# Optimization experiments

Hardware: AMD Instinct MI355X
Metric: run time of the kernel (lower is better)

## Reference

```python
import jax, jax.numpy as jnp
import numpy as np

B, L, K, D, S = 8, 1024, 1024, 128, 16  # batch, nodes, eigvecs, d_model(=d_inner), d_state
ABAR_EPS = 1e-3
BN_EPS = 1e-5


def setup_inputs() -> dict:
    key = jax.random.key(0)
    ks = jax.random.split(key, 10)
    x = jax.random.normal(ks[0], (B, L, D), jnp.float32)
    attn_mask = jnp.ones((B, L), jnp.bool_)
    EigVecs = jax.random.normal(ks[1], (B, L, K), jnp.float32)
    EigVals = jax.random.uniform(ks[2], (B, K), jnp.float32)
    # BatchNorm1d (eval mode) params
    bn_gamma = jnp.ones((D,), jnp.float32)
    bn_beta = jnp.zeros((D,), jnp.float32)
    bn_mean = jnp.zeros((D,), jnp.float32)
    bn_var = jnp.ones((D,), jnp.float32)
    # in_proj Linear(D, 2*D)
    W_in = jax.random.normal(ks[3], (D, 2 * D), jnp.float32) / np.float32(np.sqrt(D))
    b_in = jnp.zeros((2 * D,), jnp.float32)
    # SSM params
    log_Delta = np.float32(np.log(1e-3)) + np.float32(np.log(0.1) - np.log(1e-3)) * jax.random.uniform(ks[4], (1, D), jnp.float32)
    Bp = 0.01 * jax.random.normal(ks[5], (1, D, S), jnp.float32)
    Cp = 0.01 * jax.random.normal(ks[6], (1, D, S), jnp.float32)
    log_A_real = jnp.log(0.5 * jnp.ones((D, S), jnp.float32))
    A_imag = jnp.pi * jnp.broadcast_to(jnp.arange(D, dtype=jnp.float32)[:, None], (D, S))
    # out_proj Linear(D, D)
    W_out = jax.random.normal(ks[7], (D, D), jnp.float32) / np.float32(np.sqrt(D))
    b_out = jnp.zeros((D,), jnp.float32)
    return {
        "x": x, "attn_mask": attn_mask, "EigVecs": EigVecs, "EigVals": EigVals,
        "bn_gamma": bn_gamma, "bn_beta": bn_beta, "bn_mean": bn_mean, "bn_var": bn_var,
        "W_in": W_in, "b_in": b_in, "log_Delta": log_Delta, "Bp": Bp, "Cp": Cp,
        "log_A_real": log_A_real, "A_imag": A_imag, "W_out": W_out, "b_out": b_out,
    }


def reference(x, attn_mask, EigVecs, EigVals, bn_gamma, bn_beta, bn_mean, bn_var,
              W_in, b_in, log_Delta, Bp, Cp, log_A_real, A_imag, W_out, b_out):
    # --- eig preprocessing ---
    ev = 1.0 - EigVals[:, :, None, None]            # (B,K,1,1)
    ev = jnp.nan_to_num(ev)
    Q = jnp.nan_to_num(EigVecs)                      # (B,L,K)
    Q = Q / jnp.linalg.norm(Q, axis=-1, keepdims=True)
    Q = jnp.nan_to_num(Q)
    # --- in_proj: BatchNorm1d (eval) + Linear ---
    xb = (x - bn_mean) * (bn_gamma / jnp.sqrt(bn_var + BN_EPS)) + bn_beta
    h = xb @ W_in + b_in                             # (B,L,2D)
    x1, z = jnp.split(h, 2, axis=-1)                 # split [d_model, d_model]
    u = x1 * jax.nn.silu(z)                          # (B,L,D)
    # --- discretized SSM params ---
    delta = jnp.exp(log_Delta)                       # (1,D)
    A = -jnp.exp(log_A_real) + 1j * A_imag           # (D,S) complex
    Abar = jnp.exp(-ABAR_EPS + delta[..., None] * A) # (1,D,S) complex
    Bbar = delta[..., None] * Bp                     # (1,D,S)
    # --- graph Fourier transform ---
    QTX = jnp.einsum('blk,bld->bkd', Q, u)           # (B,K,D)
    QTXB = QTX[..., None] * Bbar                     # (B,K,D,S)
    lamA = ev * Abar[:, None]                        # (B,K,D,S) complex
    lamQ = jnp.real(lamA / (1.0 - lamA) * QTXB)      # A_complex & not BC_complex -> .real
    # --- inverse transform + C reduction (fused) ---
    yssm = jnp.einsum('blk,bkds,ds->bld', Q, lamQ, Cp[0])  # (B,L,D)
    y = jax.nn.silu(yssm) @ W_out + b_out
    return y
```

## Files before the change

### kernel.cpp

```cpp
#include <hip/hip_runtime.h>
#include <math.h>

#define B_ 8
#define L_ 1024
#define K_ 1024
#define D_ 128
#define S_ 16
#define DS_ (D_ * S_)
#define KS_ 4
#define CSL_ 256
#define NIT_ 8

typedef short bf16x8 __attribute__((ext_vector_type(8)));
typedef float f32x4 __attribute__((ext_vector_type(4)));
typedef __attribute__((address_space(1))) const unsigned int gu32;
typedef __attribute__((address_space(3))) unsigned int lu32;

__device__ inline unsigned short f2bf(float f) {
    unsigned int u = __float_as_uint(f);
    u = (u + 0x7fffu + ((u >> 16) & 1u)) >> 16;
    return (unsigned short)u;
}
__device__ inline float bf2f(unsigned short h) {
    return __uint_as_float(((unsigned int)h) << 16);
}

__global__ void k_params(const float* __restrict__ log_Delta,
                         const float* __restrict__ Bp,
                         const float* __restrict__ Cp,
                         const float* __restrict__ log_A_real,
                         const float* __restrict__ A_imag,
                         float* __restrict__ par) {
    int i = blockIdx.x * blockDim.x + threadIdx.x;
    if (i >= DS_) return;
    int d = i >> 4;
    int s = i & 15;
    double delta = exp((double)log_Delta[d]);
    double Are = -exp((double)log_A_real[i]);
    double Aim = (double)A_imag[i];
    double mag = exp(-1e-3 + delta * Are);
    double ang = delta * Aim;
    int o = s * D_ + d;
    par[o]            = (float)(mag * cos(ang));
    par[DS_ + o]      = (float)(mag * sin(ang));
    par[2 * DS_ + o]  = (float)(delta * (double)Bp[i] * (double)Cp[i]);
}

__global__ __launch_bounds__(256) void k_rownorm(const float* __restrict__ E,
                                                 float* __restrict__ rn) {
    int row = blockIdx.x;
    const float4* p = (const float4*)(E + (size_t)row * K_);
    int t = threadIdx.x;
    float4 v = p[t];
    float s = v.x * v.x + v.y * v.y + v.z * v.z + v.w * v.w;
    #pragma unroll
    for (int off = 32; off > 0; off >>= 1) s += __shfl_down(s, off, 64);
    __shared__ float red[4];
    if ((t & 63) == 0) red[t >> 6] = s;
    __syncthreads();
    if (t == 0) rn[row] = 1.0f / sqrtf(red[0] + red[1] + red[2] + red[3]);
}

__global__ __launch_bounds__(256) void k_inproj(
    const float* __restrict__ x, const float* __restrict__ g,
    const float* __restrict__ beta, const float* __restrict__ mean,
    const float* __restrict__ var, const float* __restrict__ W_in,
    const float* __restrict__ b_in, const float* __restrict__ rn,
    unsigned short* __restrict__ uTh, unsigned short* __restrict__ uTl) {
    __shared__ float xb[16][128];
    int row0 = blockIdx.x * 16;
    int t = threadIdx.x;
    #pragma unroll
    for (int p = 0; p < 8; ++p) {
        int idx = t + p * 256;
        int dd = idx & 127, r = idx >> 7;
        float sc = g[dd] / sqrtf(var[dd] + 1e-5f);
        xb[r][dd] = (x[(size_t)(row0 + r) * D_ + dd] - mean[dd]) * sc + beta[dd];
    }
    __syncthreads();
    int j = t & 127, half = t >> 7;
    float acc1[8], acc2[8];
    #pragma unroll
    for (int r = 0; r < 8; ++r) { acc1[r] = 0.f; acc2[r] = 0.f; }
    #pragma unroll 4
    for (int dd = 0; dd < 128; ++dd) {
        float w1 = W_in[dd * 256 + j];
        float w2 = W_in[dd * 256 + 128 + j];
        #pragma unroll
        for (int r = 0; r < 8; ++r) {
            float xv = xb[half * 8 + r][dd];
            acc1[r] = fmaf(xv, w1, acc1[r]);
            acc2[r] = fmaf(xv, w2, acc2[r]);
        }
    }
    float b1 = b_in[j], b2 = b_in[128 + j];
    bf16x8 hv, lv;
    #pragma unroll
    for (int r = 0; r < 8; ++r) {
        int row = row0 + half * 8 + r;
        float x1 = acc1[r] + b1;
        float z  = acc2[r] + b2;
        float sig = 1.0f / (1.0f + __expf(-z));
        float uv = rn[row] * x1 * z * sig;
        unsigned short h = f2bf(uv);
        hv[r] = (short)h;
        lv[r] = (short)f2bf(uv - bf2f(h));
    }
    int b = row0 >> 10;
    int l0 = (row0 & 1023) + half * 8;
    size_t off = ((size_t)b * 128 + j) * 1024 + l0;
    *(bf16x8*)&uTh[off] = hv;
    *(bf16x8*)&uTl[off] = lv;
}

template<bool ATRANS>
__global__ __launch_bounds__(256, 1) void k_gemm(
    const float* __restrict__ Asrc,
    const unsigned short* __restrict__ BsrcH,
    const unsigned short* __restrict__ BsrcL,
    float* __restrict__ P) {
    __shared__ unsigned short sAh[2][128 * 40];
    __shared__ unsigned short sAl[2][128 * 40];
    __shared__ unsigned short sBh[2][4096];
    __shared__ unsigned short sBl[2][4096];
    int bx = blockIdx.x;
    int ks = bx & (KS_ - 1);
    int mt8 = (bx >> 2) & 7;
    int b = bx >> 5;
    int m0 = mt8 * 128;
    int cbase = ks * CSL_;
    const float* Ab = Asrc + (size_t)b * 1024 * 1024;
    const unsigned short* BbH = BsrcH + (size_t)b * 128 * 1024;
    const unsigned short* BbL = BsrcL + (size_t)b * 128 * 1024;
    int t = threadIdx.x;
    int wave = t >> 6, lane = t & 63;
    int fr = lane & 15, q = lane >> 4;
    int wm = (wave & 1) * 64, wn = (wave >> 1) * 64;
    f32x4 acc[4][4];
    #pragma unroll
    for (int i = 0; i < 4; ++i)
        #pragma unroll
        for (int j = 0; j < 4; ++j) acc[i][j] = (f32x4){0.f, 0.f, 0.f, 0.f};

    float ar16[16];
    {
        int cb = cbase;
        if (ATRANS) {
            int m = t & 127, gh = (t >> 7) * 2;
            #pragma unroll
            for (int g2 = 0; g2 < 2; ++g2) {
                int g = gh + g2;
                #pragma unroll
                for (int i = 0; i < 8; ++i)
                    ar16[g2 * 8 + i] = Ab[(size_t)(cb + g * 8 + i) * 1024 + m0 + m];
            }
            #pragma unroll
            for (int g2 = 0; g2 < 2; ++g2) {
                int g = gh + g2;
                bf16x8 hv, lv;
                #pragma unroll
                for (int i = 0; i < 8; ++i) {
                    unsigned short h = f2bf(ar16[g2 * 8 + i]);
                    hv[i] = (short)h;
                    lv[i] = (short)f2bf(ar16[g2 * 8 + i] - bf2f(h));
                }
                *(bf16x8*)&sAh[0][m * 40 + g * 8] = hv;
                *(bf16x8*)&sAl[0][m * 40 + g * 8] = lv;
            }
        } else {
            #pragma unroll
            for (int p = 0; p < 4; ++p) {
                int m = (t >> 3) + p * 32, c4 = (t & 7) * 4;
                float4 v = *(const float4*)&Ab[(size_t)(m0 + m) * 1024 + cb + c4];
                float vv[4] = {v.x, v.y, v.z, v.w};
                unsigned short hs[4], ls[4];
                #pragma unroll
                for (int i = 0; i < 4; ++i) {
                    hs[i] = f2bf(vv[i]);
                    ls[i] = f2bf(vv[i] - bf2f(hs[i]));
                }
                int off = m * 40 + c4;
                *(uint2*)&sAh[0][off] = (uint2){(unsigned)hs[0] | ((unsigned)hs[1] << 16),
                                                (unsigned)hs[2] | ((unsigned)hs[3] << 16)};
                *(uint2*)&sAl[0][off] = (uint2){(unsigned)ls[0] | ((unsigned)ls[1] << 16),
                                                (unsigned)ls[2] | ((unsigned)ls[3] << 16)};
            }
        }
        #pragma unroll
        for (int j = 0; j < 2; ++j) {
            int s = wave * 2 + j;
            int qq = s >> 1, nh = (s & 1) * 64;
            const unsigned short* gh = BbH + (size_t)(nh + lane) * 1024 + cb + qq * 8;
            const unsigned short* gl = BbL + (size_t)(nh + lane) * 1024 + cb + qq * 8;
            __builtin_amdgcn_global_load_lds((gu32*)gh, (lu32*)&sBh[0][qq * 1024 + nh * 8], 16, 0, 0);
            __builtin_amdgcn_global_load_lds((gu32*)gl, (lu32*)&sBl[0][qq * 1024 + nh * 8], 16, 0, 0);
        }
    }
    __syncthreads();

    for (int it = 0; it < NIT_; ++it) {
        int cur = it & 1, nxt = cur ^ 1;
        int cb = cbase + (it + 1) * 32;
        bool pre = (it + 1 < NIT_);
        if (pre) {
            if (ATRANS) {
                int m = t & 127, gh = (t >> 7) * 2;
                #pragma unroll
                for (int g2 = 0; g2 < 2; ++g2) {
                    int g = gh + g2;
                    #pragma unroll
                    for (int i = 0; i < 8; ++i)
                        ar16[g2 * 8 + i] = Ab[(size_t)(cb + g * 8 + i) * 1024 + m0 + m];
                }
            } else {
                #pragma unroll
                for (int p = 0; p < 4; ++p) {
                    int m = (t >> 3) + p * 32, c4 = (t & 7) * 4;
                    *(float4*)&ar16[p * 4] =
                        *(const float4*)&Ab[(size_t)(m0 + m) * 1024 + cb + c4];
                }
            }
            #pragma unroll
            for (int j = 0; j < 2; ++j) {
                int s = wave * 2 + j;
                int qq = s >> 1, nh = (s & 1) * 64;
                const unsigned short* gh = BbH + (size_t)(nh + lane) * 1024 + cb + qq * 8;
                const unsigned short* gl = BbL + (size_t)(nh + lane) * 1024 + cb + qq * 8;
                __builtin_amdgcn_global_load_lds((gu32*)gh, (lu32*)&sBh[nxt][qq * 1024 + nh * 8], 16, 0, 0);
                __builtin_amdgcn_global_load_lds((gu32*)gl, (lu32*)&sBl[nxt][qq * 1024 + nh * 8], 16, 0, 0);
            }
        }
        bf16x8 ah[4], al[4], bh[4], bl[4];
        #pragma unroll
        for (int mt = 0; mt < 4; ++mt) {
            int off = (wm + mt * 16 + fr) * 40 + q * 8;
            ah[mt] = *(const bf16x8*)&sAh[cur][off];
            al[mt] = *(const bf16x8*)&sAl[cur][off];
        }
        #pragma unroll
        for (int nt = 0; nt < 4; ++nt) {
            int off = q * 1024 + (wn + nt * 16 + fr) * 8;
            bh[nt] = *(const bf16x8*)&sBh[cur][off];
            bl[nt] = *(const bf16x8*)&sBl[cur][off];
        }
        #pragma unroll
        for (int mt = 0; mt < 4; ++mt)
            #pragma unroll
            for (int nt = 0; nt < 4; ++nt) {
                acc[mt][nt] = __builtin_amdgcn_mfma_f32_16x16x32_bf16(
                    ah[mt], bh[nt], acc[mt][nt], 0, 0, 0);
                acc[mt][nt] = __builtin_amdgcn_mfma_f32_16x16x32_bf16(
                    ah[mt], bl[nt], acc[mt][nt], 0, 0, 0);
                acc[mt][nt] = __builtin_amdgcn_mfma_f32_16x16x32_bf16(
                    al[mt], bh[nt], acc[mt][nt], 0, 0, 0);
            }
        if (pre) {
            if (ATRANS) {
                int m = t & 127, gh = (t >> 7) * 2;
                #pragma unroll
                for (int g2 = 0; g2 < 2; ++g2) {
                    int g = gh + g2;
                    bf16x8 hv, lv;
                    #pragma unroll
                    for (int i = 0; i < 8; ++i) {
                        unsigned short h = f2bf(ar16[g2 * 8 + i]);
                        hv[i] = (short)h;
                        lv[i] = (short)f2bf(ar16[g2 * 8 + i] - bf2f(h));
                    }
                    *(bf16x8*)&sAh[nxt][m * 40 + g * 8] = hv;
                    *(bf16x8*)&sAl[nxt][m * 40 + g * 8] = lv;
                }
            } else {
                #pragma unroll
                for (int p = 0; p < 4; ++p) {
                    int m = (t >> 3) + p * 32, c4 = (t & 7) * 4;
                    unsigned short hs[4], ls[4];
                    #pragma unroll
                    for (int i = 0; i < 4; ++i) {
                        float v = ar16[p * 4 + i];
                        hs[i] = f2bf(v);
                        ls[i] = f2bf(v - bf2f(hs[i]));
                    }
                    int off = m * 40 + c4;
                    *(uint2*)&sAh[nxt][off] = (uint2){(unsigned)hs[0] | ((unsigned)hs[1] << 16),
                                                      (unsigned)hs[2] | ((unsigned)hs[3] << 16)};
                    *(uint2*)&sAl[nxt][off] = (uint2){(unsigned)ls[0] | ((unsigned)ls[1] << 16),
                                                      (unsigned)ls[2] | ((unsigned)ls[3] << 16)};
                }
            }
        }
        __syncthreads();
    }
    float* Pb = P + ((size_t)(ks * B_ + b) * 1024 + m0) * 128;
    #pragma unroll
    for (int mt = 0; mt < 4; ++mt)
        #pragma unroll
        for (int nt = 0; nt < 4; ++nt) {
            int col = wn + nt * 16 + fr;
            #pragma unroll
            for (int r = 0; r < 4; ++r)
                Pb[(size_t)(wm + mt * 16 + q * 4 + r) * 128 + col] = acc[mt][nt][r];
        }
}

__global__ __launch_bounds__(256) void k_gepi(
    const float* __restrict__ P, const float* __restrict__ EigVals,
    const float* __restrict__ par,
    unsigned short* __restrict__ GTh, unsigned short* __restrict__ GTl) {
    __shared__ float parS[3 * DS_];
    __shared__ float Gs[16][132];
    int t = threadIdx.x;
    for (int i = t; i < 3 * DS_; i += 256) parS[i] = par[i];
    __syncthreads();
    int bx = blockIdx.x;
    int kt = bx & 63, b = bx >> 6;
    int k0 = kt * 16;
    #pragma unroll
    for (int sub = 0; sub < 2; ++sub) {
        int k = (t >> 5) + sub * 8;
        int d4 = (t & 31) * 4;
        int row = b * 1024 + k0 + k;
        float4 s = {0.f, 0.f, 0.f, 0.f};
        #pragma unroll
        for (int sl = 0; sl < KS_; ++sl) {
            float4 v = *(const float4*)&P[((size_t)sl * 8192 + row) * 128 + d4];
            s.x += v.x; s.y += v.y; s.z += v.z; s.w += v.w;
        }
        float ev = 1.0f - EigVals[row];
        float qv[4] = {s.x, s.y, s.z, s.w};
        float o[4];
        #pragma unroll
        for (int c = 0; c < 4; ++c) {
            int dd = d4 + c;
            float w = 0.f;
            #pragma unroll
            for (int ss = 0; ss < S_; ++ss) {
                float arp = parS[ss * D_ + dd];
                float aip = parS[DS_ + ss * D_ + dd];
                float cc  = parS[2 * DS_ + ss * D_ + dd];
                float a = ev * arp, bi = ev * aip;
                float oma = 1.0f - a;
                float b2 = bi * bi;
                float num = fmaf(a, oma, -b2);
                float den = fmaf(oma, oma, b2);
                float r = __builtin_amdgcn_rcpf(den);
                r = r * (2.0f - den * r);
                w = fmaf(cc, num * r, w);
            }
            o[c] = qv[c] * w;
        }
        *(float4*)&Gs[k][d4] = (float4){o[0], o[1], o[2], o[3]};
    }
    __syncthreads();
    int d = t >> 1, kc = (t & 1) * 8;
    bf16x8 hv, lv;
    #pragma unroll
    for (int i = 0; i < 8; ++i) {
        float v = Gs[kc + i][d];
        unsigned short h = f2bf(v);
        hv[i] = (short)h;
        lv[i] = (short)f2bf(v - bf2f(h));
    }
    size_t off = ((size_t)b * 128 + d) * 1024 + k0 + kc;
    *(bf16x8*)&GTh[off] = hv;
    *(bf16x8*)&GTl[off] = lv;
}

__global__ __launch_bounds__(256) void k_out(
    const float* __restrict__ P, const float* __restrict__ rn,
    const float* __restrict__ W_out, const float* __restrict__ b_out,
    float* __restrict__ y) {
    __shared__ float Ys[16][128];
    int row0 = blockIdx.x * 16;
    int t = threadIdx.x;
    #pragma unroll
    for (int r = 0; r < 2; ++r) {
        int idx = t + r * 256;
        int rr = idx >> 5, d4 = (idx & 31) * 4;
        int grow = row0 + rr;
        float4 s = {0.f, 0.f, 0.f, 0.f};
        #pragma unroll
        for (int sl = 0; sl < KS_; ++sl) {
            float4 v = *(const float4*)&P[((size_t)sl * 8192 + grow) * 128 + d4];
            s.x += v.x; s.y += v.y; s.z += v.z; s.w += v.w;
        }
        float rv = rn[grow];
        float o[4] = {s.x * rv, s.y * rv, s.z * rv, s.w * rv};
        #pragma unroll
        for (int c = 0; c < 4; ++c) {
            float sig = 1.0f / (1.0f + __expf(-o[c]));
            Ys[rr][d4 + c] = o[c] * sig;
        }
    }
    __syncthreads();
    int j = t & 127, h = t >> 7;
    float a2[8];
    #pragma unroll
    for (int r = 0; r < 8; ++r) a2[r] = 0.f;
    for (int dd = 0; dd < 128; dd += 4) {
        float w0 = W_out[(dd + 0) * 128 + j];
        float w1 = W_out[(dd + 1) * 128 + j];
        float w2 = W_out[(dd + 2) * 128 + j];
        float w3 = W_out[(dd + 3) * 128 + j];
        #pragma unroll
        for (int r = 0; r < 8; ++r) {
            float4 yv = *(float4*)&Ys[h * 8 + r][dd];
            a2[r] = fmaf(yv.x, w0, a2[r]);
            a2[r] = fmaf(yv.y, w1, a2[r]);
            a2[r] = fmaf(yv.z, w2, a2[r]);
            a2[r] = fmaf(yv.w, w3, a2[r]);
        }
    }
    float bo = b_out[j];
    #pragma unroll
    for (int r = 0; r < 8; ++r)
        y[(size_t)(row0 + h * 8 + r) * D_ + j] = a2[r] + bo;
}

extern "C" void kernel_launch(void* const* d_in, const int* in_sizes, int n_in,
                              void* d_out, int out_size, void* d_ws, size_t ws_size,
                              hipStream_t stream) {
    const float* x          = (const float*)d_in[0];
    const float* EigVecs    = (const float*)d_in[2];
    const float* EigVals    = (const float*)d_in[3];
    const float* bn_gamma   = (const float*)d_in[4];
    const float* bn_beta    = (const float*)d_in[5];
    const float* bn_mean    = (const float*)d_in[6];
    const float* bn_var     = (const float*)d_in[7];
    const float* W_in       = (const float*)d_in[8];
    const float* b_in       = (const float*)d_in[9];
    const float* log_Delta  = (const float*)d_in[10];
    const float* Bp         = (const float*)d_in[11];
    const float* Cp         = (const float*)d_in[12];
    const float* log_A_real = (const float*)d_in[13];
    const float* A_imag     = (const float*)d_in[14];
    const float* W_out      = (const float*)d_in[15];
    const float* b_out      = (const float*)d_in[16];

    float* y = (float*)d_out;
    char* w = (char*)d_ws;
    float* rn            = (float*)(w);
    float* par           = (float*)(w + 32768);
    unsigned short* uTh  = (unsigned short*)(w + 65536);
    unsigned short* uTl  = (unsigned short*)(w + 65536 + (1u << 21));
    unsigned short* GTh  = (unsigned short*)(w + 65536 + 2 * (1u << 21));
    unsigned short* GTl  = (unsigned short*)(w + 65536 + 3 * (1u << 21));
    float* P             = (float*)(w + 65536 + 4 * (1u << 21));

    k_params<<<dim3(8), dim3(256), 0, stream>>>(log_Delta, Bp, Cp, log_A_real, A_imag, par);
    k_rownorm<<<dim3(B_ * L_), dim3(256), 0, stream>>>(EigVecs, rn);
    k_inproj<<<dim3(B_ * L_ / 16), dim3(256), 0, stream>>>(
        x, bn_gamma, bn_beta, bn_mean, bn_var, W_in, b_in, rn, uTh, uTl);
    k_gemm<true><<<dim3(B_ * 8 * KS_), dim3(256), 0, stream>>>(EigVecs, uTh, uTl, P);
    k_gepi<<<dim3(B_ * 64), dim3(256), 0, stream>>>(P, EigVals, par, GTh, GTl);
    k_gemm<false><<<dim3(B_ * 8 * KS_), dim3(256), 0, stream>>>(EigVecs, GTh, GTl, P);
    k_out<<<dim3(B_ * L_ / 16), dim3(256), 0, stream>>>(P, rn, W_out, b_out, y);
}
```

Baseline: 184.9 us.

## Halve GEMM M-tile, pre-swizzle B operand layout, drop double buffering for occupancy

The split-bf16 GEMM tile drops from 128x128 to 64x128 per block, doubling the grid to 512 blocks. Launch bounds now allow two blocks per CU, and the LDS double buffering and register prefetch are removed in favour of single-buffered loads. The producer kernels write the B operands (u and G) in a pre-swizzled chunked layout, so each global_load_lds reads contiguous 16-byte-per-lane data, and the A tile in LDS uses a rotated-column swizzle to avoid bank conflicts. The aim is more occupancy and latency hiding across blocks instead of software pipelining within a block. The cost is more redundant B-tile traffic and exposed load latency inside each block.

```diff
diff --git a/kernel.cpp b/kernel.cpp
--- a/kernel.cpp
+++ b/kernel.cpp
@@ -23,6 +23,10 @@
 }
 __device__ inline float bf2f(unsigned short h) {
     return __uint_as_float(((unsigned int)h) << 16);
+}
+
+__device__ inline size_t bswz(int b, int c, int n) {
+    return ((((size_t)b * 32 + (c >> 5)) * 4 + ((c >> 3) & 3)) * 128 + n) * 8;
 }
 
 __global__ void k_params(const float* __restrict__ log_Delta,
@@ -66,7 +70,7 @@
     const float* __restrict__ beta, const float* __restrict__ mean,
     const float* __restrict__ var, const float* __restrict__ W_in,
     const float* __restrict__ b_in, const float* __restrict__ rn,
-    unsigned short* __restrict__ uTh, unsigned short* __restrict__ uTl) {
+    unsigned short* __restrict__ uswH, unsigned short* __restrict__ uswL) {
     __shared__ float xb[16][128];
     int row0 = blockIdx.x * 16;
     int t = threadIdx.x;
@@ -108,145 +112,106 @@
     }
     int b = row0 >> 10;
     int l0 = (row0 & 1023) + half * 8;
-    size_t off = ((size_t)b * 128 + j) * 1024 + l0;
-    *(bf16x8*)&uTh[off] = hv;
-    *(bf16x8*)&uTl[off] = lv;
+    size_t off = bswz(b, l0, j);
+    *(bf16x8*)&uswH[off] = hv;
+    *(bf16x8*)&uswL[off] = lv;
 }
 
 template<bool ATRANS>
-__global__ __launch_bounds__(256, 1) void k_gemm(
+__global__ __launch_bounds__(256, 2) void k_gemm(
     const float* __restrict__ Asrc,
     const unsigned short* __restrict__ BsrcH,
     const unsigned short* __restrict__ BsrcL,
     float* __restrict__ P) {
-    __shared__ unsigned short sAh[2][128 * 40];
-    __shared__ unsigned short sAl[2][128 * 40];
-    __shared__ unsigned short sBh[2][4096];
-    __shared__ unsigned short sBl[2][4096];
+    __shared__ unsigned short sAh[64 * 40];
+    __shared__ unsigned short sAl[64 * 40];
+    __shared__ unsigned short sBh[4224];
+    __shared__ unsigned short sBl[4224];
     int bx = blockIdx.x;
     int ks = bx & (KS_ - 1);
-    int mt8 = (bx >> 2) & 7;
-    int b = bx >> 5;
-    int m0 = mt8 * 128;
+    int mt16 = (bx >> 2) & 15;
+    int b = bx >> 6;
+    int m0 = mt16 * 64;
     int cbase = ks * CSL_;
     const float* Ab = Asrc + (size_t)b * 1024 * 1024;
-    const unsigned short* BbH = BsrcH + (size_t)b * 128 * 1024;
-    const unsigned short* BbL = BsrcL + (size_t)b * 128 * 1024;
     int t = threadIdx.x;
     int wave = t >> 6, lane = t & 63;
     int fr = lane & 15, q = lane >> 4;
-    int wm = (wave & 1) * 64, wn = (wave >> 1) * 64;
-    f32x4 acc[4][4];
+    int wn = wave * 32;
+    f32x4 acc[4][2];
     #pragma unroll
     for (int i = 0; i < 4; ++i)
         #pragma unroll
-        for (int j = 0; j < 4; ++j) acc[i][j] = (f32x4){0.f, 0.f, 0.f, 0.f};
-
-    float ar16[16];
-    {
-        int cb = cbase;
+        for (int j = 0; j < 2; ++j) acc[i][j] = (f32x4){0.f, 0.f, 0.f, 0.f};
+
+    for (int it = 0; it < NIT_; ++it) {
+        int cb = cbase + it * 32;
         if (ATRANS) {
-            int m = t & 127, gh = (t >> 7) * 2;
-            #pragma unroll
-            for (int g2 = 0; g2 < 2; ++g2) {
-                int g = gh + g2;
-                #pragma unroll
-                for (int i = 0; i < 8; ++i)
-                    ar16[g2 * 8 + i] = Ab[(size_t)(cb + g * 8 + i) * 1024 + m0 + m];
-            }
-            #pragma unroll
-            for (int g2 = 0; g2 < 2; ++g2) {
-                int g = gh + g2;
-                bf16x8 hv, lv;
-                #pragma unroll
-                for (int i = 0; i < 8; ++i) {
-                    unsigned short h = f2bf(ar16[g2 * 8 + i]);
-                    hv[i] = (short)h;
-                    lv[i] = (short)f2bf(ar16[g2 * 8 + i] - bf2f(h));
-                }
-                *(bf16x8*)&sAh[0][m * 40 + g * 8] = hv;
-                *(bf16x8*)&sAl[0][m * 40 + g * 8] = lv;
-            }
+            int m = t & 63, cg = t >> 6;
+            float v[8];
+            #pragma unroll
+            for (int i = 0; i < 8; ++i)
+                v[i] = Ab[(size_t)(cb + cg * 8 + i) * 1024 + m0 + m];
+            bf16x8 hv, lv;
+            #pragma unroll
+            for (int i = 0; i < 8; ++i) {
+                unsigned short h = f2bf(v[i]);
+                hv[i] = (short)h;
+                lv[i] = (short)f2bf(v[i] - bf2f(h));
+            }
+            int p = (cg + (m >> 3)) & 3;
+            *(bf16x8*)&sAh[m * 40 + p * 8] = hv;
+            *(bf16x8*)&sAl[m * 40 + p * 8] = lv;
         } else {
-            #pragma unroll
-            for (int p = 0; p < 4; ++p) {
-                int m = (t >> 3) + p * 32, c4 = (t & 7) * 4;
-                float4 v = *(const float4*)&Ab[(size_t)(m0 + m) * 1024 + cb + c4];
-                float vv[4] = {v.x, v.y, v.z, v.w};
-                unsigned short hs[4], ls[4];
-                #pragma unroll
-                for (int i = 0; i < 4; ++i) {
-                    hs[i] = f2bf(vv[i]);
-                    ls[i] = f2bf(vv[i] - bf2f(hs[i]));
-                }
-                int off = m * 40 + c4;
-                *(uint2*)&sAh[0][off] = (uint2){(unsigned)hs[0] | ((unsigned)hs[1] << 16),
-                                                (unsigned)hs[2] | ((unsigned)hs[3] << 16)};
-                *(uint2*)&sAl[0][off] = (uint2){(unsigned)ls[0] | ((unsigned)ls[1] << 16),
-                                                (unsigned)ls[2] | ((unsigned)ls[3] << 16)};
-            }
-        }
-        #pragma unroll
-        for (int j = 0; j < 2; ++j) {
-            int s = wave * 2 + j;
-            int qq = s >> 1, nh = (s & 1) * 64;
-            const unsigned short* gh = BbH + (size_t)(nh + lane) * 1024 + cb + qq * 8;
-            const unsigned short* gl = BbL + (size_t)(nh + lane) * 1024 + cb + qq * 8;
-            __builtin_amdgcn_global_load_lds((gu32*)gh, (lu32*)&sBh[0][qq * 1024 + nh * 8], 16, 0, 0);
-            __builtin_amdgcn_global_load_lds((gu32*)gl, (lu32*)&sBl[0][qq * 1024 + nh * 8], 16, 0, 0);
-        }
-    }
-    __syncthreads();
-
-    for (int it = 0; it < NIT_; ++it) {
-        int cur = it & 1, nxt = cur ^ 1;
-        int cb = cbase + (it + 1) * 32;
-        bool pre = (it + 1 < NIT_);
-        if (pre) {
-            if (ATRANS) {
-                int m = t & 127, gh = (t >> 7) * 2;
-                #pragma unroll
-                for (int g2 = 0; g2 < 2; ++g2) {
-                    int g = gh + g2;
-                    #pragma unroll
-                    for (int i = 0; i < 8; ++i)
-                        ar16[g2 * 8 + i] = Ab[(size_t)(cb + g * 8 + i) * 1024 + m0 + m];
-                }
-            } else {
-                #pragma unroll
-                for (int p = 0; p < 4; ++p) {
-                    int m = (t >> 3) + p * 32, c4 = (t & 7) * 4;
-                    *(float4*)&ar16[p * 4] =
-                        *(const float4*)&Ab[(size_t)(m0 + m) * 1024 + cb + c4];
-                }
-            }
-            #pragma unroll
-            for (int j = 0; j < 2; ++j) {
-                int s = wave * 2 + j;
-                int qq = s >> 1, nh = (s & 1) * 64;
-                const unsigned short* gh = BbH + (size_t)(nh + lane) * 1024 + cb + qq * 8;
-                const unsigned short* gl = BbL + (size_t)(nh + lane) * 1024 + cb + qq * 8;
-                __builtin_amdgcn_global_load_lds((gu32*)gh, (lu32*)&sBh[nxt][qq * 1024 + nh * 8], 16, 0, 0);
-                __builtin_amdgcn_global_load_lds((gu32*)gl, (lu32*)&sBl[nxt][qq * 1024 + nh * 8], 16, 0, 0);
-            }
-        }
-        bf16x8 ah[4], al[4], bh[4], bl[4];
+            int m = t >> 2, cg = t & 3;
+            float4 v0 = *(const float4*)&Ab[(size_t)(m0 + m) * 1024 + cb + cg * 8];
+            float4 v1 = *(const float4*)&Ab[(size_t)(m0 + m) * 1024 + cb + cg * 8 + 4];
+            float v[8] = {v0.x, v0.y, v0.z, v0.w, v1.x, v1.y, v1.z, v1.w};
+            bf16x8 hv, lv;
+            #pragma unroll
+            for (int i = 0; i < 8; ++i) {
+                unsigned short h = f2bf(v[i]);
+                hv[i] = (short)h;
+                lv[i] = (short)f2bf(v[i] - bf2f(h));
+            }
+            int p = (cg + (m >> 3)) & 3;
+            *(bf16x8*)&sAh[m * 40 + p * 8] = hv;
+            *(bf16x8*)&sAl[m * 40 + p * 8] = lv;
+        }
+        {
+            int ct = (cbase >> 5) + it;
+            size_t src0 = (((size_t)(b * 32 + ct)) * 4) * 1024;
+            #pragma unroll
+            for (int j = 0; j < 4; ++j) {
+                int s = wave + j * 4;
+                int qq = s & 3, nh = (s >> 2) & 1, hl = s >> 3;
+                const unsigned short* src =
+                    (hl ? BsrcL : BsrcH) + src0 + ((size_t)qq * 128 + nh * 64 + lane) * 8;
+                unsigned short* dst =
+                    (hl ? sBl : sBh) + qq * 1032 + nh * 512;
+                __builtin_amdgcn_global_load_lds((gu32*)src, (lu32*)dst, 16, 0, 0);
+            }
+        }
+        __syncthreads();
+        bf16x8 ah[4], al[4], bh[2], bl[2];
         #pragma unroll
         for (int mt = 0; mt < 4; ++mt) {
-            int off = (wm + mt * 16 + fr) * 40 + q * 8;
-            ah[mt] = *(const bf16x8*)&sAh[cur][off];
-            al[mt] = *(const bf16x8*)&sAl[cur][off];
-        }
-        #pragma unroll
-        for (int nt = 0; nt < 4; ++nt) {
-            int off = q * 1024 + (wn + nt * 16 + fr) * 8;
-            bh[nt] = *(const bf16x8*)&sBh[cur][off];
-            bl[nt] = *(const bf16x8*)&sBl[cur][off];
+            int r = mt * 16 + fr;
+            int p = (q + (r >> 3)) & 3;
+            int off = r * 40 + p * 8;
+            ah[mt] = *(const bf16x8*)&sAh[off];
+            al[mt] = *(const bf16x8*)&sAl[off];
+        }
+        #pragma unroll
+        for (int nt = 0; nt < 2; ++nt) {
+            int off = q * 1032 + (wn + nt * 16 + fr) * 8;
+            bh[nt] = *(const bf16x8*)&sBh[off];
+            bl[nt] = *(const bf16x8*)&sBl[off];
         }
         #pragma unroll
         for (int mt = 0; mt < 4; ++mt)
             #pragma unroll
-            for (int nt = 0; nt < 4; ++nt) {
+            for (int nt = 0; nt < 2; ++nt) {
                 acc[mt][nt] = __builtin_amdgcn_mfma_f32_16x16x32_bf16(
                     ah[mt], bh[nt], acc[mt][nt], 0, 0, 0);
                 acc[mt][nt] = __builtin_amdgcn_mfma_f32_16x16x32_bf16(
@@ -254,59 +219,24 @@
                 acc[mt][nt] = __builtin_amdgcn_mfma_f32_16x16x32_bf16(
                     al[mt], bh[nt], acc[mt][nt], 0, 0, 0);
             }
-        if (pre) {
-            if (ATRANS) {
-                int m = t & 127, gh = (t >> 7) * 2;
-                #pragma unroll
-                for (int g2 = 0; g2 < 2; ++g2) {
-                    int g = gh + g2;
-                    bf16x8 hv, lv;
-                    #pragma unroll
-                    for (int i = 0; i < 8; ++i) {
-                        unsigned short h = f2bf(ar16[g2 * 8 + i]);
-                        hv[i] = (short)h;
-                        lv[i] = (short)f2bf(ar16[g2 * 8 + i] - bf2f(h));
-                    }
-                    *(bf16x8*)&sAh[nxt][m * 40 + g * 8] = hv;
-                    *(bf16x8*)&sAl[nxt][m * 40 + g * 8] = lv;
-                }
-            } else {
-                #pragma unroll
-                for (int p = 0; p < 4; ++p) {
-                    int m = (t >> 3) + p * 32, c4 = (t & 7) * 4;
-                    unsigned short hs[4], ls[4];
-                    #pragma unroll
-                    for (int i = 0; i < 4; ++i) {
-                        float v = ar16[p * 4 + i];
-                        hs[i] = f2bf(v);
-                        ls[i] = f2bf(v - bf2f(hs[i]));
-                    }
-                    int off = m * 40 + c4;
-                    *(uint2*)&sAh[nxt][off] = (uint2){(unsigned)hs[0] | ((unsigned)hs[1] << 16),
-                                                      (unsigned)hs[2] | ((unsigned)hs[3] << 16)};
-                    *(uint2*)&sAl[nxt][off] = (uint2){(unsigned)ls[0] | ((unsigned)ls[1] << 16),
-                                                      (unsigned)ls[2] | ((unsigned)ls[3] << 16)};
-                }
-            }
-        }
         __syncthreads();
     }
     float* Pb = P + ((size_t)(ks * B_ + b) * 1024 + m0) * 128;
     #pragma unroll
     for (int mt = 0; mt < 4; ++mt)
         #pragma unroll
-        for (int nt = 0; nt < 4; ++nt) {
+        for (int nt = 0; nt < 2; ++nt) {
             int col = wn + nt * 16 + fr;
             #pragma unroll
             for (int r = 0; r < 4; ++r)
-                Pb[(size_t)(wm + mt * 16 + q * 4 + r) * 128 + col] = acc[mt][nt][r];
+                Pb[(size_t)(mt * 16 + q * 4 + r) * 128 + col] = acc[mt][nt][r];
         }
 }
 
 __global__ __launch_bounds__(256) void k_gepi(
     const float* __restrict__ P, const float* __restrict__ EigVals,
     const float* __restrict__ par,
-    unsigned short* __restrict__ GTh, unsigned short* __restrict__ GTl) {
+    unsigned short* __restrict__ GswH, unsigned short* __restrict__ GswL) {
     __shared__ float parS[3 * DS_];
     __shared__ float Gs[16][132];
     int t = threadIdx.x;
@@ -361,9 +291,9 @@
         hv[i] = (short)h;
         lv[i] = (short)f2bf(v - bf2f(h));
     }
-    size_t off = ((size_t)b * 128 + d) * 1024 + k0 + kc;
-    *(bf16x8*)&GTh[off] = hv;
-    *(bf16x8*)&GTl[off] = lv;
+    size_t off = bswz(b, k0 + kc, d);
+    *(bf16x8*)&GswH[off] = hv;
+    *(bf16x8*)&GswL[off] = lv;
 }
 
 __global__ __launch_bounds__(256) void k_out(
@@ -441,18 +371,18 @@
     char* w = (char*)d_ws;
     float* rn            = (float*)(w);
     float* par           = (float*)(w + 32768);
-    unsigned short* uTh  = (unsigned short*)(w + 65536);
-    unsigned short* uTl  = (unsigned short*)(w + 65536 + (1u << 21));
-    unsigned short* GTh  = (unsigned short*)(w + 65536 + 2 * (1u << 21));
-    unsigned short* GTl  = (unsigned short*)(w + 65536 + 3 * (1u << 21));
+    unsigned short* uswH = (unsigned short*)(w + 65536);
+    unsigned short* uswL = (unsigned short*)(w + 65536 + (1u << 21));
+    unsigned short* GswH = (unsigned short*)(w + 65536 + 2 * (1u << 21));
+    unsigned short* GswL = (unsigned short*)(w + 65536 + 3 * (1u << 21));
     float* P             = (float*)(w + 65536 + 4 * (1u << 21));
 
     k_params<<<dim3(8), dim3(256), 0, stream>>>(log_Delta, Bp, Cp, log_A_real, A_imag, par);
     k_rownorm<<<dim3(B_ * L_), dim3(256), 0, stream>>>(EigVecs, rn);
     k_inproj<<<dim3(B_ * L_ / 16), dim3(256), 0, stream>>>(
-        x, bn_gamma, bn_beta, bn_mean, bn_var, W_in, b_in, rn, uTh, uTl);
-    k_gemm<true><<<dim3(B_ * 8 * KS_), dim3(256), 0, stream>>>(EigVecs, uTh, uTl, P);
-    k_gepi<<<dim3(B_ * 64), dim3(256), 0, stream>>>(P, EigVals, par, GTh, GTl);
-    k_gemm<false><<<dim3(B_ * 8 * KS_), dim3(256), 0, stream>>>(EigVecs, GTh, GTl, P);
+        x, bn_gamma, bn_beta, bn_mean, bn_var, W_in, b_in, rn, uswH, uswL);
+    k_gemm<true><<<dim3(16 * KS_ * B_), dim3(256), 0, stream>>>(EigVecs, uswH, uswL, P);
+    k_gepi<<<dim3(B_ * 64), dim3(256), 0, stream>>>(P, EigVals, par, GswH, GswL);
+    k_gemm<false><<<dim3(16 * KS_ * B_), dim3(256), 0, stream>>>(EigVecs, GswH, GswL, P);
     k_out<<<dim3(B_ * L_ / 16), dim3(256), 0, stream>>>(P, rn, W_out, b_out, y);
 }
```

Result: faster. 179.4 us (-3.0%).
